# Optimization experiments

Measured on AMD Instinct MI355X. Metric: run time of the kernel, lower is better.

Reference implementation:

```python
import jax, jax.numpy as jnp
import numpy as np

# module hyperparameters (from init_kwargs)
STRIDE, PAD, DIL = 1, 1, 1
GROUPS, DG = 1, 1
KH, KW = 3, 3
CIN, COUT = 256, 256


def _mdcn_forward(x, offset, mask, weight, bias):
    B, C, H, W = x.shape
    Cout = weight.shape[0]
    K = KH * KW
    Ho = (H + 2 * PAD - (DIL * (KH - 1) + 1)) // STRIDE + 1
    Wo = (W + 2 * PAD - (DIL * (KW - 1) + 1)) // STRIDE + 1
    Cg = C // DG

    # offset channel layout: ((g*K + k)*2 + {0: dy, 1: dx})
    off = offset.reshape(B, DG, KH, KW, 2, Ho, Wo)
    base_y = (jnp.arange(Ho) * STRIDE - PAD)[None, :] + DIL * jnp.arange(KH)[:, None]  # [KH,Ho]
    base_x = (jnp.arange(Wo) * STRIDE - PAD)[None, :] + DIL * jnp.arange(KW)[:, None]  # [KW,Wo]
    sy = base_y[None, None, :, None, :, None].astype(x.dtype) + off[:, :, :, :, 0]  # [B,DG,KH,KW,Ho,Wo]
    sx = base_x[None, None, None, :, None, :].astype(x.dtype) + off[:, :, :, :, 1]

    y0f = jnp.floor(sy); x0f = jnp.floor(sx)
    wy = sy - y0f; wx = sx - x0f
    y0 = y0f.astype(jnp.int32); x0 = x0f.astype(jnp.int32)

    xg = x.reshape(B, DG, Cg, H * W)

    def corner(yc, xc, w):
        valid = (yc >= 0) & (yc < H) & (xc >= 0) & (xc < W)
        idx = jnp.clip(yc, 0, H - 1) * W + jnp.clip(xc, 0, W - 1)  # [B,DG,KH,KW,Ho,Wo]
        v = jnp.take_along_axis(xg, idx.reshape(B, DG, 1, -1), axis=3)  # [B,DG,Cg,K*Ho*Wo]
        v = v.reshape(B, DG, Cg, KH, KW, Ho, Wo)
        return v * (w * valid.astype(x.dtype))[:, :, None]

    val = (corner(y0, x0, (1 - wy) * (1 - wx))
           + corner(y0, x0 + 1, (1 - wy) * wx)
           + corner(y0 + 1, x0, wy * (1 - wx))
           + corner(y0 + 1, x0 + 1, wy * wx))  # [B,DG,Cg,KH,KW,Ho,Wo]

    cols = val * mask.reshape(B, DG, 1, KH, KW, Ho, Wo)
    cols = cols.reshape(B, GROUPS, (C // GROUPS) * K, Ho * Wo)
    wg = weight.reshape(GROUPS, Cout // GROUPS, (C // GROUPS) * K)
    out = jnp.einsum('gok,bgkp->bgop', wg, cols).reshape(B, Cout, Ho, Wo)
    return out + bias[None, :, None, None]


def setup_inputs() -> dict:
    key = jax.random.key(0)
    k1, k2, k3, k4 = jax.random.split(key, 4)
    B, H, W = 4, 64, 64
    x = jax.random.normal(k1, (B, CIN, H, W), dtype=jnp.float32)
    offset = jax.random.normal(k2, (B, 2 * DG * KH * KW, H, W), dtype=jnp.float32)
    mask = jax.random.uniform(k3, (B, DG * KH * KW, H, W), dtype=jnp.float32)
    stdv = 1.0 / np.sqrt(CIN * KH * KW)
    weight = jax.random.uniform(k4, (COUT, CIN // GROUPS, KH, KW), dtype=jnp.float32,
                                minval=-stdv, maxval=stdv)
    bias = jnp.zeros((COUT,), dtype=jnp.float32)
    return {"x": x, "offset": offset, "mask": mask, "weight": weight, "bias": bias}


def reference(x, offset, mask, weight, bias):
    return _mdcn_forward(x, offset, mask, weight, bias)
```

## Files before the change

kernel.cpp:

```cpp
#include <hip/hip_runtime.h>
#include <hip/hip_bf16.h>
#include <stdint.h>

#define KDIM 2304

typedef __bf16 bf16_t;
typedef bf16_t bf16x8 __attribute__((ext_vector_type(8)));
typedef float f32x4 __attribute__((ext_vector_type(4)));
typedef float f32x2 __attribute__((ext_vector_type(2)));

__device__ __forceinline__ float b2f_lo(uint32_t u) {
  union { uint32_t i; float f; } c; c.i = u << 16; return c.f;
}
__device__ __forceinline__ float b2f_hi(uint32_t u) {
  union { uint32_t i; float f; } c; c.i = u & 0xffff0000u; return c.f;
}
__device__ __forceinline__ uint32_t pk_bf16(float a, float b) {
  __hip_bfloat162 h = __float22bfloat162_rn(make_float2(a, b));
  union { __hip_bfloat162 h; uint32_t u; } c; c.h = h; return c.u;
}

__device__ __forceinline__ void g2lds16(const uint16_t* g, uint16_t* l) {
  __builtin_amdgcn_global_load_lds((const __attribute__((address_space(1))) void*)g,
                                   (__attribute__((address_space(3))) void*)l,
                                   16, 0, 0);
}

__global__ __launch_bounds__(256) void k_prep(const float* __restrict__ x,
                                              uint16_t* __restrict__ xt,
                                              const float* __restrict__ w,
                                              uint16_t* __restrict__ wt) {
  int tid = threadIdx.x;
  if (blockIdx.x < 2048) {
    __shared__ float tile[32][65];
    int b = blockIdx.x >> 9;
    int cgrp = (blockIdx.x >> 6) & 7;
    int sgrp = blockIdx.x & 63;
    int c0 = cgrp << 5, s0 = sgrp << 6;
#pragma unroll
    for (int it = 0; it < 2; ++it) {
      int f = tid + it * 256;
      int rr = f >> 4, col = (f & 15) << 2;
      float4 v = *(const float4*)&x[((size_t)(b * 256 + c0 + rr)) * 4096 + s0 + col];
      tile[rr][col + 0] = v.x;
      tile[rr][col + 1] = v.y;
      tile[rr][col + 2] = v.z;
      tile[rr][col + 3] = v.w;
    }
    __syncthreads();
    int sp = tid >> 2, cg = tid & 3;
    uint4 o;
    o.x = pk_bf16(tile[cg * 8 + 0][sp], tile[cg * 8 + 1][sp]);
    o.y = pk_bf16(tile[cg * 8 + 2][sp], tile[cg * 8 + 3][sp]);
    o.z = pk_bf16(tile[cg * 8 + 4][sp], tile[cg * 8 + 5][sp]);
    o.w = pk_bf16(tile[cg * 8 + 6][sp], tile[cg * 8 + 7][sp]);
    *(uint4*)&xt[((size_t)b * 4096 + s0 + sp) * 256 + c0 + cg * 8] = o;
  } else {
    __shared__ float wl[2304];
    int cout = blockIdx.x - 2048;
    const float* wrow = w + (size_t)cout * 2304;
    for (int i = tid; i < 576; i += 256)
      *(float4*)&wl[i * 4] = *(const float4*)&wrow[i * 4];
    __syncthreads();
    uint16_t* wdst = wt + (size_t)cout * KDIM + tid;
#pragma unroll
    for (int t = 0; t < 9; ++t)
      wdst[t * 256] = (uint16_t)(pk_bf16(wl[tid * 9 + t], 0.f) & 0xffffu);
  }
}

__device__ __forceinline__ void mk_corners(int tap, int p, int ho,
                                           const float* s_off, const float* s_msk,
                                           const uint16_t* xtb,
                                           float cw[4], const uint16_t* cp[4]) {
  int kh = tap / 3, kw = tap - kh * 3;
  float dy = s_off[(2 * tap) * 64 + p];
  float dx = s_off[(2 * tap + 1) * 64 + p];
  float mm = s_msk[tap * 64 + p];
  float sy = (float)(ho - 1 + kh) + dy;
  float sx = (float)(p - 1 + kw) + dx;
  float fy = floorf(sy), fx = floorf(sx);
  int y0 = (int)fy, x0 = (int)fx;
  float wy = sy - fy, wx = sx - fx;
#pragma unroll
  for (int cy = 0; cy < 2; ++cy) {
#pragma unroll
    for (int cx = 0; cx < 2; ++cx) {
      int y = y0 + cy, xx = x0 + cx;
      float wgt = (cy ? wy : 1.f - wy) * (cx ? wx : 1.f - wx) * mm;
      bool v = ((unsigned)y < 64u) && ((unsigned)xx < 64u);
      wgt = v ? wgt : 0.f;
      int yc = min(max(y, 0), 63), xc = min(max(xx, 0), 63);
      cw[cy * 2 + cx] = wgt;
      cp[cy * 2 + cx] = xtb + ((yc << 6) + xc) * 256;
    }
  }
}

__device__ __forceinline__ uint4 blend4(const uint4 d[4], const float cw[4]) {
  f32x2 f0 = {0.f, 0.f}, f1 = {0.f, 0.f}, f2 = {0.f, 0.f}, f3 = {0.f, 0.f};
#pragma unroll
  for (int c = 0; c < 4; ++c) {
    f32x2 wc = {cw[c], cw[c]};
    f0 += wc * f32x2{b2f_lo(d[c].x), b2f_hi(d[c].x)};
    f1 += wc * f32x2{b2f_lo(d[c].y), b2f_hi(d[c].y)};
    f2 += wc * f32x2{b2f_lo(d[c].z), b2f_hi(d[c].z)};
    f3 += wc * f32x2{b2f_lo(d[c].w), b2f_hi(d[c].w)};
  }
  uint4 o;
  o.x = pk_bf16(f0.x, f0.y);
  o.y = pk_bf16(f1.x, f1.y);
  o.z = pk_bf16(f2.x, f2.y);
  o.w = pk_bf16(f3.x, f3.y);
  return o;
}

__global__ __launch_bounds__(512, 2) void k_fused(const uint16_t* __restrict__ xt,
                                                  const uint16_t* __restrict__ wt,
                                                  const float* __restrict__ off,
                                                  const float* __restrict__ msk,
                                                  const float* __restrict__ bias,
                                                  float* __restrict__ out) {
  __shared__ __align__(16) uint16_t As[2][2][256][32];
  __shared__ __align__(16) uint16_t Bs[2][2][64][32];
  __shared__ float s_off[18 * 64];
  __shared__ float s_msk[9 * 64];

  int tid = threadIdx.x;
  int b = blockIdx.x >> 6, ho = blockIdx.x & 63;

  const float* offb = off + (size_t)b * 18 * 4096 + ho * 64;
  for (int i = tid; i < 18 * 64; i += 512)
    s_off[i] = offb[(size_t)(i >> 6) * 4096 + (i & 63)];
  const float* mskb = msk + (size_t)b * 9 * 4096 + ho * 64;
  for (int i = tid; i < 9 * 64; i += 512)
    s_msk[i] = mskb[(size_t)(i >> 6) * 4096 + (i & 63)];

  int lane = tid & 63, wv = tid >> 6;
  int wm = wv >> 1, wn = wv & 1;
  int q = lane >> 4, r = lane & 15;

  int p = tid >> 3, cg = tid & 7;
  const uint16_t* xtb = xt + (size_t)b * 4096 * 256 + cg * 8;
  int bsub = cg >> 2, bcol = (cg & 3) * 8;

  int asub = wv & 1, arow0 = (wv >> 1) * 64;
  const uint16_t* abase = wt + (size_t)(arow0 + (lane >> 2)) * KDIM + asub * 32 + (lane & 3) * 8;

  f32x4 acc[4][2];
#pragma unroll
  for (int i = 0; i < 4; ++i)
#pragma unroll
    for (int j = 0; j < 2; ++j) acc[i][j] = f32x4{0.f, 0.f, 0.f, 0.f};

  __syncthreads();

  float cw[4];
  const uint16_t* cp[4];

  mk_corners(0, p, ho, s_off, s_msk, xtb, cw, cp);
  {
    uint4 d0[4];
#pragma unroll
    for (int c = 0; c < 4; ++c) d0[c] = *(const uint4*)(cp[c]);
#pragma unroll
    for (int j = 0; j < 4; ++j)
      g2lds16(abase + (size_t)(j * 16) * KDIM, &As[0][asub][arow0 + j * 16][0]);
    uint4 o = blend4(d0, cw);
    *(uint4*)&Bs[0][bsub][p][bcol] = o;
  }

  for (int i = 0; i < 36; ++i) {
    int cur = i & 1;
    __syncthreads();
    uint4 dn[4];
    if (i != 35) {
      int nx = i + 1;
      if ((nx & 3) == 0) mk_corners(nx >> 2, p, ho, s_off, s_msk, xtb, cw, cp);
      int ofs = (nx & 3) * 64;
#pragma unroll
      for (int c = 0; c < 4; ++c) dn[c] = *(const uint4*)(cp[c] + ofs);
      int ofsK = (nx >> 2) * 256 + (nx & 3) * 64;
      int nb = nx & 1;
#pragma unroll
      for (int j = 0; j < 4; ++j)
        g2lds16(abase + ofsK + (size_t)(j * 16) * KDIM, &As[nb][asub][arow0 + j * 16][0]);
    }
    bf16x8 af[4][2], bfr[2][2];
#pragma unroll
    for (int kh = 0; kh < 2; ++kh) {
#pragma unroll
      for (int mi = 0; mi < 4; ++mi)
        af[mi][kh] = *(const bf16x8*)&As[cur][kh][wm * 64 + mi * 16 + r][q * 8];
#pragma unroll
      for (int ni = 0; ni < 2; ++ni)
        bfr[ni][kh] = *(const bf16x8*)&Bs[cur][kh][wn * 32 + ni * 16 + r][q * 8];
    }
#pragma unroll
    for (int kh = 0; kh < 2; ++kh)
#pragma unroll
      for (int mi = 0; mi < 4; ++mi)
#pragma unroll
        for (int ni = 0; ni < 2; ++ni)
          acc[mi][ni] = __builtin_amdgcn_mfma_f32_16x16x32_bf16(af[mi][kh], bfr[ni][kh], acc[mi][ni], 0, 0, 0);
    if (i != 35) {
      uint4 o = blend4(dn, cw);
      *(uint4*)&Bs[(i + 1) & 1][bsub][p][bcol] = o;
    }
  }

#pragma unroll
  for (int mi = 0; mi < 4; ++mi) {
#pragma unroll
    for (int j = 0; j < 4; ++j) {
      int m = wm * 64 + mi * 16 + q * 4 + j;
      float bv = bias[m];
#pragma unroll
      for (int ni = 0; ni < 2; ++ni) {
        int wo = wn * 32 + ni * 16 + r;
        out[((size_t)(b * 256 + m)) * 4096 + ho * 64 + wo] = acc[mi][ni][j] + bv;
      }
    }
  }
}

extern "C" void kernel_launch(void* const* d_in, const int* in_sizes, int n_in,
                              void* d_out, int out_size, void* d_ws, size_t ws_size,
                              hipStream_t stream) {
  (void)in_sizes; (void)n_in; (void)out_size; (void)ws_size;
  const float* x      = (const float*)d_in[0];
  const float* offset = (const float*)d_in[1];
  const float* mask   = (const float*)d_in[2];
  const float* weight = (const float*)d_in[3];
  const float* bias   = (const float*)d_in[4];
  float* out = (float*)d_out;

  uint8_t* ws = (uint8_t*)d_ws;
  uint16_t* xt = (uint16_t*)ws;
  uint16_t* wt = (uint16_t*)(ws + 8388608);

  k_prep<<<dim3(2304), 256, 0, stream>>>(x, xt, weight, wt);
  k_fused<<<dim3(256), 512, 0, stream>>>(xt, wt, offset, mask, bias, out);
}
```

Measured before the change: 132.2 us.

## Split each output row across two 256-thread blocks and read offsets directly

The fused kernel now gives each block half an output row (32 pixels) with 256 threads, so the grid doubles from 256 to 512 blocks. This fills more of the GPU's compute units. Offset and mask values are now read straight from global memory in mk_corners instead of being staged in shared memory, which drops the initial barrier. In exchange, each block reloads the full weight tile for only 32 pixels, which doubles weight traffic per output, and the offset reads are less coalesced.

```diff
diff --git a/kernel.cpp b/kernel.cpp
--- a/kernel.cpp
+++ b/kernel.cpp
@@ -69,16 +69,18 @@
   }
 }
 
-__device__ __forceinline__ void mk_corners(int tap, int p, int ho,
-                                           const float* s_off, const float* s_msk,
+__device__ __forceinline__ void mk_corners(int tap, int wo, int ho, int b,
+                                           const float* __restrict__ off,
+                                           const float* __restrict__ msk,
                                            const uint16_t* xtb,
                                            float cw[4], const uint16_t* cp[4]) {
   int kh = tap / 3, kw = tap - kh * 3;
-  float dy = s_off[(2 * tap) * 64 + p];
-  float dx = s_off[(2 * tap + 1) * 64 + p];
-  float mm = s_msk[tap * 64 + p];
+  size_t sp = (size_t)ho * 64 + wo;
+  float dy = off[((size_t)(b * 18 + 2 * tap)) * 4096 + sp];
+  float dx = off[((size_t)(b * 18 + 2 * tap + 1)) * 4096 + sp];
+  float mm = msk[((size_t)(b * 9 + tap)) * 4096 + sp];
   float sy = (float)(ho - 1 + kh) + dy;
-  float sx = (float)(p - 1 + kw) + dx;
+  float sx = (float)(wo - 1 + kw) + dx;
   float fy = floorf(sy), fx = floorf(sx);
   int y0 = (int)fy, x0 = (int)fx;
   float wy = sy - fy, wx = sx - fx;
@@ -115,57 +117,50 @@
   return o;
 }
 
-__global__ __launch_bounds__(512, 2) void k_fused(const uint16_t* __restrict__ xt,
+__global__ __launch_bounds__(256, 2) void k_fused(const uint16_t* __restrict__ xt,
                                                   const uint16_t* __restrict__ wt,
                                                   const float* __restrict__ off,
                                                   const float* __restrict__ msk,
                                                   const float* __restrict__ bias,
                                                   float* __restrict__ out) {
   __shared__ __align__(16) uint16_t As[2][2][256][32];
-  __shared__ __align__(16) uint16_t Bs[2][2][64][32];
-  __shared__ float s_off[18 * 64];
-  __shared__ float s_msk[9 * 64];
+  __shared__ __align__(16) uint16_t Bs[2][2][32][32];
 
   int tid = threadIdx.x;
-  int b = blockIdx.x >> 6, ho = blockIdx.x & 63;
-
-  const float* offb = off + (size_t)b * 18 * 4096 + ho * 64;
-  for (int i = tid; i < 18 * 64; i += 512)
-    s_off[i] = offb[(size_t)(i >> 6) * 4096 + (i & 63)];
-  const float* mskb = msk + (size_t)b * 9 * 4096 + ho * 64;
-  for (int i = tid; i < 9 * 64; i += 512)
-    s_msk[i] = mskb[(size_t)(i >> 6) * 4096 + (i & 63)];
+  int half = blockIdx.x & 1;
+  int ho = (blockIdx.x >> 1) & 63;
+  int b = blockIdx.x >> 7;
+  int w0 = half << 5;
 
   int lane = tid & 63, wv = tid >> 6;
-  int wm = wv >> 1, wn = wv & 1;
   int q = lane >> 4, r = lane & 15;
 
   int p = tid >> 3, cg = tid & 7;
+  int wo_p = w0 + p;
   const uint16_t* xtb = xt + (size_t)b * 4096 * 256 + cg * 8;
   int bsub = cg >> 2, bcol = (cg & 3) * 8;
 
-  int asub = wv & 1, arow0 = (wv >> 1) * 64;
-  const uint16_t* abase = wt + (size_t)(arow0 + (lane >> 2)) * KDIM + asub * 32 + (lane & 3) * 8;
+  const uint16_t* abase = wt + (size_t)(wv * 64 + (lane >> 2)) * KDIM + (lane & 3) * 8;
 
   f32x4 acc[4][2];
 #pragma unroll
   for (int i = 0; i < 4; ++i)
 #pragma unroll
     for (int j = 0; j < 2; ++j) acc[i][j] = f32x4{0.f, 0.f, 0.f, 0.f};
-
-  __syncthreads();
 
   float cw[4];
   const uint16_t* cp[4];
 
-  mk_corners(0, p, ho, s_off, s_msk, xtb, cw, cp);
+  mk_corners(0, wo_p, ho, b, off, msk, xtb, cw, cp);
   {
     uint4 d0[4];
 #pragma unroll
     for (int c = 0; c < 4; ++c) d0[c] = *(const uint4*)(cp[c]);
 #pragma unroll
-    for (int j = 0; j < 4; ++j)
-      g2lds16(abase + (size_t)(j * 16) * KDIM, &As[0][asub][arow0 + j * 16][0]);
+    for (int s = 0; s < 2; ++s)
+#pragma unroll
+      for (int j = 0; j < 4; ++j)
+        g2lds16(abase + s * 32 + (size_t)(j * 16) * KDIM, &As[0][s][wv * 64 + j * 16][0]);
     uint4 o = blend4(d0, cw);
     *(uint4*)&Bs[0][bsub][p][bcol] = o;
   }
@@ -176,33 +171,36 @@
     uint4 dn[4];
     if (i != 35) {
       int nx = i + 1;
-      if ((nx & 3) == 0) mk_corners(nx >> 2, p, ho, s_off, s_msk, xtb, cw, cp);
+      if ((nx & 3) == 0) mk_corners(nx >> 2, wo_p, ho, b, off, msk, xtb, cw, cp);
       int ofs = (nx & 3) * 64;
 #pragma unroll
       for (int c = 0; c < 4; ++c) dn[c] = *(const uint4*)(cp[c] + ofs);
       int ofsK = (nx >> 2) * 256 + (nx & 3) * 64;
       int nb = nx & 1;
 #pragma unroll
-      for (int j = 0; j < 4; ++j)
-        g2lds16(abase + ofsK + (size_t)(j * 16) * KDIM, &As[nb][asub][arow0 + j * 16][0]);
+      for (int s = 0; s < 2; ++s)
+#pragma unroll
+        for (int j = 0; j < 4; ++j)
+          g2lds16(abase + ofsK + s * 32 + (size_t)(j * 16) * KDIM,
+                  &As[nb][s][wv * 64 + j * 16][0]);
     }
     bf16x8 af[4][2], bfr[2][2];
 #pragma unroll
-    for (int kh = 0; kh < 2; ++kh) {
+    for (int s = 0; s < 2; ++s) {
 #pragma unroll
       for (int mi = 0; mi < 4; ++mi)
-        af[mi][kh] = *(const bf16x8*)&As[cur][kh][wm * 64 + mi * 16 + r][q * 8];
+        af[mi][s] = *(const bf16x8*)&As[cur][s][wv * 64 + mi * 16 + r][q * 8];
 #pragma unroll
       for (int ni = 0; ni < 2; ++ni)
-        bfr[ni][kh] = *(const bf16x8*)&Bs[cur][kh][wn * 32 + ni * 16 + r][q * 8];
-    }
-#pragma unroll
-    for (int kh = 0; kh < 2; ++kh)
+        bfr[ni][s] = *(const bf16x8*)&Bs[cur][s][ni * 16 + r][q * 8];
+    }
+#pragma unroll
+    for (int s = 0; s < 2; ++s)
 #pragma unroll
       for (int mi = 0; mi < 4; ++mi)
 #pragma unroll
         for (int ni = 0; ni < 2; ++ni)
-          acc[mi][ni] = __builtin_amdgcn_mfma_f32_16x16x32_bf16(af[mi][kh], bfr[ni][kh], acc[mi][ni], 0, 0, 0);
+          acc[mi][ni] = __builtin_amdgcn_mfma_f32_16x16x32_bf16(af[mi][s], bfr[ni][s], acc[mi][ni], 0, 0, 0);
     if (i != 35) {
       uint4 o = blend4(dn, cw);
       *(uint4*)&Bs[(i + 1) & 1][bsub][p][bcol] = o;
@@ -213,11 +211,11 @@
   for (int mi = 0; mi < 4; ++mi) {
 #pragma unroll
     for (int j = 0; j < 4; ++j) {
-      int m = wm * 64 + mi * 16 + q * 4 + j;
+      int m = wv * 64 + mi * 16 + q * 4 + j;
       float bv = bias[m];
 #pragma unroll
       for (int ni = 0; ni < 2; ++ni) {
-        int wo = wn * 32 + ni * 16 + r;
+        int wo = w0 + ni * 16 + r;
         out[((size_t)(b * 256 + m)) * 4096 + ho * 64 + wo] = acc[mi][ni][j] + bv;
       }
     }
@@ -240,5 +238,5 @@
   uint16_t* wt = (uint16_t*)(ws + 8388608);
 
   k_prep<<<dim3(2304), 256, 0, stream>>>(x, xt, weight, wt);
-  k_fused<<<dim3(256), 512, 0, stream>>>(xt, wt, offset, mask, bias, out);
-}
+  k_fused<<<dim3(512), 256, 0, stream>>>(xt, wt, offset, mask, bias, out);
+}
```

Result: slower. 138.4 us (+4.7%).
